# Optimization experiments

Measured on AMD Instinct MI355X. Metric: run time of the kernel, lower is better.

## Reference

```python
import jax, jax.numpy as jnp
import numpy as np

N = 50000      # nodes
E = 800000     # edges (avg degree 16)
D_IN = 128     # in_feats
D_H = 128      # n_hidden
D_OUT = 64     # n_classes


def _lin(k, fan_in, fan_out):
    # torch nn.Linear default init: U(-1/sqrt(fan_in), 1/sqrt(fan_in))
    s = 1.0 / np.sqrt(fan_in)
    return jax.random.uniform(k, (fan_in, fan_out), jnp.float32, -s, s)


def setup_inputs() -> dict:
    key = jax.random.key(0)
    ks = jax.random.split(key, 12)
    return {
        "x": jax.random.normal(ks[0], (N, D_IN), jnp.float32),
        "edge_src": jax.random.randint(ks[1], (E,), 0, N, jnp.int32),
        "edge_dst": jax.random.randint(ks[2], (E,), 0, N, jnp.int32),
        # layer 0: in_feats -> n_hidden
        "W_self0": _lin(ks[3], D_IN, D_H),
        "W_neigh0": _lin(ks[4], D_IN, D_H),
        "b0": jnp.zeros((D_H,), jnp.float32),
        # layer 1: n_hidden -> n_hidden
        "W_self1": _lin(ks[5], D_H, D_H),
        "W_neigh1": _lin(ks[6], D_H, D_H),
        "b1": jnp.zeros((D_H,), jnp.float32),
        # layer 2: n_hidden -> n_classes
        "W_self2": _lin(ks[7], D_H, D_OUT),
        "W_neigh2": _lin(ks[8], D_H, D_OUT),
        "b2": jnp.zeros((D_OUT,), jnp.float32),
    }


def _sage_conv(x, src, dst, W_self, W_neigh, b):
    """DGL SAGEConv with 'mean' aggregator:
    out = x @ W_self + mean_{u in N(v)} x_u @ W_neigh + b
    Zero in-degree nodes get zero neighbor term (degree clamped to 1)."""
    n = x.shape[0]
    agg = jax.ops.segment_sum(x[src], dst, num_segments=n)          # [N, d]
    deg = jax.ops.segment_sum(jnp.ones((src.shape[0],), x.dtype), dst,
                              num_segments=n)                        # [N]
    h_neigh = agg / jnp.maximum(deg, 1.0)[:, None]
    return x @ W_self + h_neigh @ W_neigh + b


def reference(x, edge_src, edge_dst,
              W_self0, W_neigh0, b0,
              W_self1, W_neigh1, b1,
              W_self2, W_neigh2, b2):
    # dropout is identity in eval/inference mode
    h = jax.nn.relu(_sage_conv(x, edge_src, edge_dst, W_self0, W_neigh0, b0))
    h = jax.nn.relu(_sage_conv(h, edge_src, edge_dst, W_self1, W_neigh1, b1))
    return _sage_conv(h, edge_src, edge_dst, W_self2, W_neigh2, b2)
```

## Files before the change

### kernel.cpp

```cpp
#include <hip/hip_runtime.h>

#define NN 50000
#define NPAD 50048
#define NE 800000
#define CAP 64

typedef _Float16 f16;
typedef _Float16 f16x4 __attribute__((ext_vector_type(4)));
typedef _Float16 f16x8 __attribute__((ext_vector_type(8)));
typedef float f32x4 __attribute__((ext_vector_type(4)));

__global__ __launch_bounds__(256) void cvt_x(const float* __restrict__ X,
                                             f16* __restrict__ XH, int total4) {
    int i = blockIdx.x * 256 + threadIdx.x;
    if (i < total4) {
        float4 v = *reinterpret_cast<const float4*>(X + (size_t)i * 4);
        f16x4 o = {(f16)v.x, (f16)v.y, (f16)v.z, (f16)v.w};
        *reinterpret_cast<f16x4*>(XH + (size_t)i * 4) = o;
    }
}

__global__ __launch_bounds__(256) void build_weights(
    const float* __restrict__ WS0, const float* __restrict__ WN0,
    const float* __restrict__ WS1, const float* __restrict__ WN1,
    const float* __restrict__ WS2, const float* __restrict__ WN2,
    f16* __restrict__ wt0, f16* __restrict__ wt1, f16* __restrict__ wt2) {
    int i = blockIdx.x * 256 + threadIdx.x;
    if (i < 32768) {
        int j = i >> 8, k = i & 255;
        float v = (k < 128) ? WS0[k * 128 + j] : WN0[(k - 128) * 128 + j];
        wt0[j * 256 + k] = (f16)v;
    } else if (i < 65536) {
        int t = i - 32768;
        int j = t >> 8, k = t & 255;
        float v = (k < 128) ? WS1[k * 128 + j] : WN1[(k - 128) * 128 + j];
        wt1[j * 256 + k] = (f16)v;
    } else if (i < 81920) {
        int t = i - 65536;
        int j = t >> 7, k = t & 127;
        float v = (j < 64) ? WS2[k * 64 + j] : WN2[k * 64 + (j - 64)];
        wt2[j * 128 + k] = (f16)v;
    }
}

__global__ __launch_bounds__(256) void fill_kernel(const int* __restrict__ src,
                                                   const int* __restrict__ dst,
                                                   int* __restrict__ cursor,
                                                   int* __restrict__ eidx, int E) {
    int e = blockIdx.x * 256 + threadIdx.x;
    if (e < E) {
        int d = dst[e];
        int p = atomicAdd(&cursor[d], 1);
        if (p < CAP) eidx[(d << 6) + p] = src[e];
    }
}

__global__ __launch_bounds__(256) void gather_mean4(const f16* __restrict__ X,
                                                    const int* __restrict__ cnt_,
                                                    const int* __restrict__ eidx,
                                                    f16* __restrict__ OUT, int n) {
    int wave = blockIdx.x * 4 + (threadIdx.x >> 6);
    int lane = threadIdx.x & 63;
    int node = wave * 4 + (lane >> 4);
    int sl = lane & 15;
    if (node >= n) return;
    int cnt = cnt_[node];
    const int* row = eidx + ((size_t)node << 6);
    float acc[8];
#pragma unroll
    for (int j = 0; j < 8; j++) acc[j] = 0.f;
    int e = 0;
    for (; e + 4 <= cnt; e += 4) {
        int4 s4 = *reinterpret_cast<const int4*>(row + e);
        f16x8 v0 = *reinterpret_cast<const f16x8*>(X + (size_t)s4.x * 128 + sl * 8);
        f16x8 v1 = *reinterpret_cast<const f16x8*>(X + (size_t)s4.y * 128 + sl * 8);
        f16x8 v2 = *reinterpret_cast<const f16x8*>(X + (size_t)s4.z * 128 + sl * 8);
        f16x8 v3 = *reinterpret_cast<const f16x8*>(X + (size_t)s4.w * 128 + sl * 8);
#pragma unroll
        for (int j = 0; j < 8; j++)
            acc[j] += ((float)v0[j] + (float)v1[j]) + ((float)v2[j] + (float)v3[j]);
    }
    for (; e < cnt; e++) {
        int s0 = row[e];
        f16x8 v0 = *reinterpret_cast<const f16x8*>(X + (size_t)s0 * 128 + sl * 8);
#pragma unroll
        for (int j = 0; j < 8; j++) acc[j] += (float)v0[j];
    }
    float iv = 1.0f / fmaxf((float)cnt, 1.0f);
    f16x8 o;
#pragma unroll
    for (int j = 0; j < 8; j++) o[j] = (f16)(acc[j] * iv);
    *reinterpret_cast<f16x8*>(OUT + (size_t)node * 128 + sl * 8) = o;
}

__global__ __launch_bounds__(256) void gather_out(const f16* __restrict__ Y,
                                                  const int* __restrict__ cnt_,
                                                  const int* __restrict__ eidx,
                                                  float* __restrict__ OUT, int n) {
    int wave = blockIdx.x * 4 + (threadIdx.x >> 6);
    int lane = threadIdx.x & 63;
    int node = wave * 8 + (lane >> 3);
    int sl = lane & 7;
    if (node >= n) return;
    int cnt = cnt_[node];
    const int* row = eidx + ((size_t)node << 6);
    float acc[8];
#pragma unroll
    for (int j = 0; j < 8; j++) acc[j] = 0.f;
    int e = 0;
    for (; e + 4 <= cnt; e += 4) {
        int4 s4 = *reinterpret_cast<const int4*>(row + e);
        f16x8 v0 = *reinterpret_cast<const f16x8*>(Y + (size_t)s4.x * 128 + 64 + sl * 8);
        f16x8 v1 = *reinterpret_cast<const f16x8*>(Y + (size_t)s4.y * 128 + 64 + sl * 8);
        f16x8 v2 = *reinterpret_cast<const f16x8*>(Y + (size_t)s4.z * 128 + 64 + sl * 8);
        f16x8 v3 = *reinterpret_cast<const f16x8*>(Y + (size_t)s4.w * 128 + 64 + sl * 8);
#pragma unroll
        for (int j = 0; j < 8; j++)
            acc[j] += ((float)v0[j] + (float)v1[j]) + ((float)v2[j] + (float)v3[j]);
    }
    for (; e < cnt; e++) {
        int s0 = row[e];
        f16x8 v0 = *reinterpret_cast<const f16x8*>(Y + (size_t)s0 * 128 + 64 + sl * 8);
#pragma unroll
        for (int j = 0; j < 8; j++) acc[j] += (float)v0[j];
    }
    float iv = 1.0f / fmaxf((float)cnt, 1.0f);
    f16x8 self = *reinterpret_cast<const f16x8*>(Y + (size_t)node * 128 + sl * 8);
    float o[8];
#pragma unroll
    for (int j = 0; j < 8; j++) o[j] = acc[j] * iv + (float)self[j];
    float* dst = OUT + (size_t)node * 64 + sl * 8;
    *reinterpret_cast<float4*>(dst) = *reinterpret_cast<float4*>(o);
    *reinterpret_cast<float4*>(dst + 4) = *reinterpret_cast<float4*>(o + 4);
}

template <int DOUT, int K, bool RELU, bool HALFBIAS>
__global__ __launch_bounds__(256) void mfma_gemm(const f16* __restrict__ A1,
                                                 const f16* __restrict__ A2,
                                                 const f16* __restrict__ WT,
                                                 const float* __restrict__ BIAS,
                                                 f16* __restrict__ O16, int n) {
    constexpr int MT = 4;
    constexpr int NT = 4;
    const int lane = threadIdx.x & 63;
    const int wid = threadIdx.x >> 6;
    const int m0 = blockIdx.x * 128 + (wid >> 1) * 64;
    const int n0 = (wid & 1) * 64;

    const int ar = lane & 15;
    const int kg = (lane >> 4) * 8;

    f32x4 acc[MT][NT];
#pragma unroll
    for (int mt = 0; mt < MT; mt++)
#pragma unroll
        for (int nt = 0; nt < NT; nt++) acc[mt][nt] = (f32x4){0.f, 0.f, 0.f, 0.f};

#pragma unroll
    for (int k0 = 0; k0 < K; k0 += 32) {
        const f16* Abase = (K == 256 && k0 >= 128) ? A2 : A1;
        const int kk = (k0 & 127) + kg;
        f16x8 a[MT], b[NT];
#pragma unroll
        for (int mt = 0; mt < MT; mt++)
            a[mt] = *reinterpret_cast<const f16x8*>(
                Abase + (size_t)(m0 + mt * 16 + ar) * 128 + kk);
#pragma unroll
        for (int nt = 0; nt < NT; nt++)
            b[nt] = *reinterpret_cast<const f16x8*>(
                WT + (size_t)(n0 + nt * 16 + ar) * K + k0 + kg);
#pragma unroll
        for (int mt = 0; mt < MT; mt++)
#pragma unroll
            for (int nt = 0; nt < NT; nt++)
                acc[mt][nt] = __builtin_amdgcn_mfma_f32_16x16x32_f16(
                    a[mt], b[nt], acc[mt][nt], 0, 0, 0);
    }

    const int orow = (lane >> 4) * 4;
    const int ocol = lane & 15;
#pragma unroll
    for (int nt = 0; nt < NT; nt++) {
        const int col = n0 + nt * 16 + ocol;
        const float bias = HALFBIAS ? (col < 64 ? BIAS[col] : 0.f) : BIAS[col];
#pragma unroll
        for (int mt = 0; mt < MT; mt++) {
#pragma unroll
            for (int j = 0; j < 4; j++) {
                int row = m0 + mt * 16 + orow + j;
                if (row < n) {
                    float v = acc[mt][nt][j] + bias;
                    if (RELU) v = fmaxf(v, 0.f);
                    O16[(size_t)row * DOUT + col] = (f16)v;
                }
            }
        }
    }
}

extern "C" void kernel_launch(void* const* d_in, const int* in_sizes, int n_in,
                              void* d_out, int out_size, void* d_ws, size_t ws_size,
                              hipStream_t stream) {
    const float* x        = (const float*)d_in[0];
    const int*   esrc     = (const int*)d_in[1];
    const int*   edst     = (const int*)d_in[2];
    const float* W_self0  = (const float*)d_in[3];
    const float* W_neigh0 = (const float*)d_in[4];
    const float* b0       = (const float*)d_in[5];
    const float* W_self1  = (const float*)d_in[6];
    const float* W_neigh1 = (const float*)d_in[7];
    const float* b1       = (const float*)d_in[8];
    const float* W_self2  = (const float*)d_in[9];
    const float* W_neigh2 = (const float*)d_in[10];
    const float* b2       = (const float*)d_in[11];
    float* out = (float*)d_out;

    char* ws = (char*)d_ws;
    auto align1k = [](size_t v) { return (v + 1023) & ~(size_t)1023; };
    size_t off = 0;
    int* cursor = (int*)(ws + off); off = align1k(off + (size_t)NN * 4);
    int* eidx   = (int*)(ws + off); off = align1k(off + (size_t)NN * CAP * 4);
    f16* wt0    = (f16*)(ws + off); off = align1k(off + (size_t)128 * 256 * 2);
    f16* wt1    = (f16*)(ws + off); off = align1k(off + (size_t)128 * 256 * 2);
    f16* wt2    = (f16*)(ws + off); off = align1k(off + (size_t)128 * 128 * 2);
    const size_t FEAT16 = (size_t)NPAD * 128 * 2;
    f16* xh = (f16*)(ws + off); off += FEAT16;
    f16* hm = (f16*)(ws + off); off += FEAT16;
    f16* h0 = (f16*)(ws + off); off += FEAT16;
    f16* h1 = (f16*)(ws + off); off += FEAT16;

    const int E = NE, n = NN;
    const int eblocks = (E + 255) / 256;
    const int g4blocks = (n + 15) / 16;
    const int g8blocks = (n + 31) / 32;
    const int gemm_blocks = NPAD / 128;

    hipMemsetAsync(cursor, 0, (size_t)n * sizeof(int), stream);
    fill_kernel<<<eblocks, 256, 0, stream>>>(esrc, edst, cursor, eidx, E);

    cvt_x<<<(n * 128 / 4 + 255) / 256, 256, 0, stream>>>(x, xh, n * 128 / 4);
    build_weights<<<320, 256, 0, stream>>>(W_self0, W_neigh0, W_self1, W_neigh1,
                                           W_self2, W_neigh2, wt0, wt1, wt2);

    gather_mean4<<<g4blocks, 256, 0, stream>>>(xh, cursor, eidx, hm, n);
    mfma_gemm<128, 256, true, false><<<gemm_blocks, 256, 0, stream>>>(xh, hm, wt0, b0,
                                                                      h0, n);
    gather_mean4<<<g4blocks, 256, 0, stream>>>(h0, cursor, eidx, hm, n);
    mfma_gemm<128, 256, true, false><<<gemm_blocks, 256, 0, stream>>>(h0, hm, wt1, b1,
                                                                      h1, n);
    mfma_gemm<128, 128, false, true><<<gemm_blocks, 256, 0, stream>>>(h1, nullptr, wt2,
                                                                      b2, hm, n);
    gather_out<<<g8blocks, 256, 0, stream>>>(hm, cursor, eidx, out, n);
}
```

Baseline: 210.0 us.

## Fuse prep kernels into one launch with destination-sliced edge fill; unroll gathers

Merges the edge-fill, feature conversion and weight-transposition kernels into one prep kernel, which removes two launches. The edge fill now makes 8 passes over the edge list, and each pass only handles destinations in its own node slice. The likely aim is to keep atomic and scatter writes local (e.g., in an L2/XCD slice), at the cost of reading edges 8 times. The gather kernels also gain an 8-way unrolled loop so more loads are in flight.

Result: faster. 194.7 us (-7.3%).

```diff
diff --git a/kernel.cpp b/kernel.cpp
--- a/kernel.cpp
+++ b/kernel.cpp
@@ -4,54 +4,68 @@
 #define NPAD 50048
 #define NE 800000
 #define CAP 64
+#define NSLICE 6250
+
+#define EBG 391
+#define EDGE_BLOCKS (EBG * 8)
+#define CVT_BLOCKS 782
+#define W_BLOCKS 320
+#define PREP_GRID (EDGE_BLOCKS + CVT_BLOCKS + W_BLOCKS)
 
 typedef _Float16 f16;
-typedef _Float16 f16x4 __attribute__((ext_vector_type(4)));
 typedef _Float16 f16x8 __attribute__((ext_vector_type(8)));
 typedef float f32x4 __attribute__((ext_vector_type(4)));
 
-__global__ __launch_bounds__(256) void cvt_x(const float* __restrict__ X,
-                                             f16* __restrict__ XH, int total4) {
-    int i = blockIdx.x * 256 + threadIdx.x;
-    if (i < total4) {
-        float4 v = *reinterpret_cast<const float4*>(X + (size_t)i * 4);
-        f16x4 o = {(f16)v.x, (f16)v.y, (f16)v.z, (f16)v.w};
-        *reinterpret_cast<f16x4*>(XH + (size_t)i * 4) = o;
-    }
-}
-
-__global__ __launch_bounds__(256) void build_weights(
+__global__ __launch_bounds__(256) void prep_kernel(
+    const float* __restrict__ X, const int* __restrict__ esrc,
+    const int* __restrict__ edst,
     const float* __restrict__ WS0, const float* __restrict__ WN0,
     const float* __restrict__ WS1, const float* __restrict__ WN1,
     const float* __restrict__ WS2, const float* __restrict__ WN2,
-    f16* __restrict__ wt0, f16* __restrict__ wt1, f16* __restrict__ wt2) {
-    int i = blockIdx.x * 256 + threadIdx.x;
-    if (i < 32768) {
-        int j = i >> 8, k = i & 255;
-        float v = (k < 128) ? WS0[k * 128 + j] : WN0[(k - 128) * 128 + j];
-        wt0[j * 256 + k] = (f16)v;
-    } else if (i < 65536) {
-        int t = i - 32768;
-        int j = t >> 8, k = t & 255;
-        float v = (k < 128) ? WS1[k * 128 + j] : WN1[(k - 128) * 128 + j];
-        wt1[j * 256 + k] = (f16)v;
-    } else if (i < 81920) {
-        int t = i - 65536;
-        int j = t >> 7, k = t & 127;
-        float v = (j < 64) ? WS2[k * 64 + j] : WN2[k * 64 + (j - 64)];
-        wt2[j * 128 + k] = (f16)v;
-    }
-}
-
-__global__ __launch_bounds__(256) void fill_kernel(const int* __restrict__ src,
-                                                   const int* __restrict__ dst,
-                                                   int* __restrict__ cursor,
-                                                   int* __restrict__ eidx, int E) {
-    int e = blockIdx.x * 256 + threadIdx.x;
-    if (e < E) {
-        int d = dst[e];
-        int p = atomicAdd(&cursor[d], 1);
-        if (p < CAP) eidx[(d << 6) + p] = src[e];
+    f16* __restrict__ XH, f16* __restrict__ wt0, f16* __restrict__ wt1,
+    f16* __restrict__ wt2, int* __restrict__ cursor, int* __restrict__ eidx) {
+    const int bid = blockIdx.x;
+    if (bid < EDGE_BLOCKS) {
+        const int g = bid & 7;
+        const int gi = bid >> 3;
+        const int lo = g * NSLICE, hi = lo + NSLICE;
+        const int per = (NE + EBG - 1) / EBG;
+        const int s = gi * per;
+        const int e_end = (s + per < NE) ? s + per : NE;
+        for (int e = s + threadIdx.x; e < e_end; e += 256) {
+            int d = edst[e];
+            if (d >= lo && d < hi) {
+                int p = atomicAdd(&cursor[d], 1);
+                if (p < CAP) eidx[(d << 6) + p] = esrc[e];
+            }
+        }
+    } else if (bid < EDGE_BLOCKS + CVT_BLOCKS) {
+        const int total8 = NN * 128 / 8;
+        int t = (bid - EDGE_BLOCKS) * 256 + threadIdx.x;
+        for (int i = t; i < total8; i += CVT_BLOCKS * 256) {
+            float4 v0 = *reinterpret_cast<const float4*>(X + (size_t)i * 8);
+            float4 v1 = *reinterpret_cast<const float4*>(X + (size_t)i * 8 + 4);
+            f16x8 o = {(f16)v0.x, (f16)v0.y, (f16)v0.z, (f16)v0.w,
+                       (f16)v1.x, (f16)v1.y, (f16)v1.z, (f16)v1.w};
+            *reinterpret_cast<f16x8*>(XH + (size_t)i * 8) = o;
+        }
+    } else {
+        int t = (bid - EDGE_BLOCKS - CVT_BLOCKS) * 256 + threadIdx.x;
+        if (t < 32768) {
+            int j = t >> 8, k = t & 255;
+            float v = (k < 128) ? WS0[k * 128 + j] : WN0[(k - 128) * 128 + j];
+            wt0[j * 256 + k] = (f16)v;
+        } else if (t < 65536) {
+            int u = t - 32768;
+            int j = u >> 8, k = u & 255;
+            float v = (k < 128) ? WS1[k * 128 + j] : WN1[(k - 128) * 128 + j];
+            wt1[j * 256 + k] = (f16)v;
+        } else if (t < 81920) {
+            int u = t - 65536;
+            int j = u >> 7, k = u & 127;
+            float v = (j < 64) ? WS2[k * 64 + j] : WN2[k * 64 + (j - 64)];
+            wt2[j * 128 + k] = (f16)v;
+        }
     }
 }
 
@@ -70,6 +84,22 @@
 #pragma unroll
     for (int j = 0; j < 8; j++) acc[j] = 0.f;
     int e = 0;
+    for (; e + 8 <= cnt; e += 8) {
+        int4 sa = *reinterpret_cast<const int4*>(row + e);
+        int4 sb = *reinterpret_cast<const int4*>(row + e + 4);
+        f16x8 v0 = *reinterpret_cast<const f16x8*>(X + (size_t)sa.x * 128 + sl * 8);
+        f16x8 v1 = *reinterpret_cast<const f16x8*>(X + (size_t)sa.y * 128 + sl * 8);
+        f16x8 v2 = *reinterpret_cast<const f16x8*>(X + (size_t)sa.z * 128 + sl * 8);
+        f16x8 v3 = *reinterpret_cast<const f16x8*>(X + (size_t)sa.w * 128 + sl * 8);
+        f16x8 v4 = *reinterpret_cast<const f16x8*>(X + (size_t)sb.x * 128 + sl * 8);
+        f16x8 v5 = *reinterpret_cast<const f16x8*>(X + (size_t)sb.y * 128 + sl * 8);
+        f16x8 v6 = *reinterpret_cast<const f16x8*>(X + (size_t)sb.z * 128 + sl * 8);
+        f16x8 v7 = *reinterpret_cast<const f16x8*>(X + (size_t)sb.w * 128 + sl * 8);
+#pragma unroll
+        for (int j = 0; j < 8; j++)
+            acc[j] += (((float)v0[j] + (float)v1[j]) + ((float)v2[j] + (float)v3[j])) +
+                      (((float)v4[j] + (float)v5[j]) + ((float)v6[j] + (float)v7[j]));
+    }
     for (; e + 4 <= cnt; e += 4) {
         int4 s4 = *reinterpret_cast<const int4*>(row + e);
         f16x8 v0 = *reinterpret_cast<const f16x8*>(X + (size_t)s4.x * 128 + sl * 8);
@@ -108,6 +138,22 @@
 #pragma unroll
     for (int j = 0; j < 8; j++) acc[j] = 0.f;
     int e = 0;
+    for (; e + 8 <= cnt; e += 8) {
+        int4 sa = *reinterpret_cast<const int4*>(row + e);
+        int4 sb = *reinterpret_cast<const int4*>(row + e + 4);
+        f16x8 v0 = *reinterpret_cast<const f16x8*>(Y + (size_t)sa.x * 128 + 64 + sl * 8);
+        f16x8 v1 = *reinterpret_cast<const f16x8*>(Y + (size_t)sa.y * 128 + 64 + sl * 8);
+        f16x8 v2 = *reinterpret_cast<const f16x8*>(Y + (size_t)sa.z * 128 + 64 + sl * 8);
+        f16x8 v3 = *reinterpret_cast<const f16x8*>(Y + (size_t)sa.w * 128 + 64 + sl * 8);
+        f16x8 v4 = *reinterpret_cast<const f16x8*>(Y + (size_t)sb.x * 128 + 64 + sl * 8);
+        f16x8 v5 = *reinterpret_cast<const f16x8*>(Y + (size_t)sb.y * 128 + 64 + sl * 8);
+        f16x8 v6 = *reinterpret_cast<const f16x8*>(Y + (size_t)sb.z * 128 + 64 + sl * 8);
+        f16x8 v7 = *reinterpret_cast<const f16x8*>(Y + (size_t)sb.w * 128 + 64 + sl * 8);
+#pragma unroll
+        for (int j = 0; j < 8; j++)
+            acc[j] += (((float)v0[j] + (float)v1[j]) + ((float)v2[j] + (float)v3[j])) +
+                      (((float)v4[j] + (float)v5[j]) + ((float)v6[j] + (float)v7[j]));
+    }
     for (; e + 4 <= cnt; e += 4) {
         int4 s4 = *reinterpret_cast<const int4*>(row + e);
         f16x8 v0 = *reinterpret_cast<const f16x8*>(Y + (size_t)s4.x * 128 + 64 + sl * 8);
@@ -229,18 +275,16 @@
     f16* h0 = (f16*)(ws + off); off += FEAT16;
     f16* h1 = (f16*)(ws + off); off += FEAT16;
 
-    const int E = NE, n = NN;
-    const int eblocks = (E + 255) / 256;
+    const int n = NN;
     const int g4blocks = (n + 15) / 16;
     const int g8blocks = (n + 31) / 32;
     const int gemm_blocks = NPAD / 128;
 
     hipMemsetAsync(cursor, 0, (size_t)n * sizeof(int), stream);
-    fill_kernel<<<eblocks, 256, 0, stream>>>(esrc, edst, cursor, eidx, E);
-
-    cvt_x<<<(n * 128 / 4 + 255) / 256, 256, 0, stream>>>(x, xh, n * 128 / 4);
-    build_weights<<<320, 256, 0, stream>>>(W_self0, W_neigh0, W_self1, W_neigh1,
-                                           W_self2, W_neigh2, wt0, wt1, wt2);
+    prep_kernel<<<PREP_GRID, 256, 0, stream>>>(x, esrc, edst,
+                                               W_self0, W_neigh0, W_self1, W_neigh1,
+                                               W_self2, W_neigh2,
+                                               xh, wt0, wt1, wt2, cursor, eidx);
 
     gather_mean4<<<g4blocks, 256, 0, stream>>>(xh, cursor, eidx, hm, n);
     mfma_gemm<128, 256, true, false><<<gemm_blocks, 256, 0, stream>>>(xh, hm, wt0, b0,
```
